# Kernel optimization log

Hardware: AMD Instinct MI355X
Metric: run time of the kernel (lower is better)

The kernel has to match this reference:

```python
import jax, jax.numpy as jnp
import numpy as np

B, N, C_IN, C_OUT, HID = 2, 512, 16, 16, 64


def setup_inputs() -> dict:
    key = jax.random.key(0)
    ks = jax.random.split(key, 6)
    return {
        "features": jax.random.normal(ks[0], (B, N, C_IN), dtype=jnp.float32),
        "geometry": jax.random.normal(ks[1], (B, N, 3), dtype=jnp.float32),
        "W1": jax.random.normal(ks[2], (HID, 4), dtype=jnp.float32) * 0.5,
        "b1": jax.random.normal(ks[3], (HID,), dtype=jnp.float32) * 0.1,
        "W2": jax.random.normal(ks[4], (C_OUT * C_IN, HID), dtype=jnp.float32) * 0.1,
        "b2": jax.random.normal(ks[5], (C_OUT * C_IN,), dtype=jnp.float32) * 0.1,
    }


def reference(features, geometry, W1, b1, W2, b2):
    # rb = geometry.unsqueeze(1) -> [z,1,b,xyz]; ra = geometry.unsqueeze(2) -> [z,a,1,xyz]
    rel = geometry[:, None, :, :] - geometry[:, :, None, :]  # [z, a, b, 3] = rb - ra
    # kernel network: MLP on (rel, |rel|) -> [z, a, b, C_out, C_in]
    r2 = jnp.sum(rel * rel, axis=-1, keepdims=True)
    norm = jnp.sqrt(r2 + 1e-12)                              # differentiable at 0
    feat = jnp.concatenate([rel, norm], axis=-1)             # [z, a, b, 4]
    h = jax.nn.gelu(jnp.einsum('zabf,hf->zabh', feat, W1) + b1)
    k = (jnp.einsum('zabh,oh->zabo', h, W2) + b2)            # [z, a, b, C_out*C_in]
    z, a, b = k.shape[:3]
    k = k.reshape(z, a, b, C_OUT, C_IN)
    # contraction: torch.einsum('zabij,zbj->zabi')
    return jnp.einsum('zabij,zbj->zabi', k, features)
```

## Files before the change

### kernel.cpp

```cpp
#include <hip/hip_runtime.h>

#define NQ   512
#define CI   16
#define CO   16
#define HIDN 64

typedef __attribute__((ext_vector_type(8))) short bf16x8;
typedef __attribute__((ext_vector_type(4))) float f32x4;
typedef __attribute__((ext_vector_type(4))) unsigned u32x4;
typedef __attribute__((ext_vector_type(2))) unsigned u32x2;

__device__ __forceinline__ unsigned cvt_pk_bf16(float a, float b) {
    unsigned r;
    asm("v_cvt_pk_bf16_f32 %0, %1, %2" : "=v"(r) : "v"(a), "v"(b));
    return r;
}

__global__ __launch_bounds__(256, 4) void fused_mfma_kernel(
    const float* __restrict__ features,
    const float* __restrict__ geometry,
    const float* __restrict__ W1,
    const float* __restrict__ b1,
    const float* __restrict__ W2,
    const float* __restrict__ b2,
    float* __restrict__ out)
{
    __shared__ __attribute__((aligned(16))) unsigned short Mhi[CO * HIDN];
    __shared__ __attribute__((aligned(16))) unsigned short Mlo[CO * HIDN];
    __shared__ __attribute__((aligned(16))) float W1_sm[HIDN * 4];
    __shared__ float b1_sm[HIDN];
    __shared__ float c_sm[CO];
    __shared__ float f_sm[CI];

    const int bid = blockIdx.x;
    const int zb  = bid >> 1;
    const int a0  = (bid & 1) << 8;
    const int z   = zb >> 9;
    const int b   = zb & 511;
    const int tid = threadIdx.x;

    W1_sm[tid] = W1[tid];
    if (tid < HIDN) b1_sm[tid] = b1[tid];
    if (tid < CI)   f_sm[tid]  = features[zb * CI + tid];
    __syncthreads();

    const int wv    = tid >> 6;
    const int lane  = tid & 63;
    const int col   = lane & 15;
    const int g     = lane >> 4;
    const int abase = a0 + wv * 64;

    const float gbx = geometry[(z * NQ + b) * 3 + 0];
    const float gby = geometry[(z * NQ + b) * 3 + 1];
    const float gbz = geometry[(z * NQ + b) * 3 + 2];
    float rel[4][4];
    #pragma unroll
    for (int t = 0; t < 4; ++t) {
        const float* ga = geometry + (size_t)(z * NQ + abase + t * 16 + col) * 3;
        float rx = gbx - ga[0], ry = gby - ga[1], rz = gbz - ga[2];
        rel[t][0] = rx; rel[t][1] = ry; rel[t][2] = rz;
        rel[t][3] = sqrtf(fmaf(rx, rx, fmaf(ry, ry, rz * rz)) + 1e-12f);
    }

    {
        const int i  = tid >> 4;
        const int k4 = (tid & 15) << 2;
        f32x4 m = {0.f, 0.f, 0.f, 0.f};
        #pragma unroll
        for (int j = 0; j < CI; ++j) {
            const f32x4 w2 = *reinterpret_cast<const f32x4*>(&W2[(i * CI + j) * HIDN + k4]);
            const float fj = f_sm[j];
            #pragma unroll
            for (int p = 0; p < 4; ++p) m[p] = fmaf(fj, w2[p], m[p]);
        }
        const unsigned h0 = cvt_pk_bf16(m[0], m[1]);
        const unsigned h1 = cvt_pk_bf16(m[2], m[3]);
        const float f0 = __builtin_bit_cast(float, h0 << 16);
        const float f1 = __builtin_bit_cast(float, h0 & 0xffff0000u);
        const float f2 = __builtin_bit_cast(float, h1 << 16);
        const float f3 = __builtin_bit_cast(float, h1 & 0xffff0000u);
        const unsigned l0 = cvt_pk_bf16(m[0] - f0, m[1] - f1);
        const unsigned l1 = cvt_pk_bf16(m[2] - f2, m[3] - f3);
        const int bir = (k4 << 1) ^ ((i & 7) << 4);
        *reinterpret_cast<u32x2*>(reinterpret_cast<char*>(Mhi) + i * 128 + bir) = (u32x2){h0, h1};
        *reinterpret_cast<u32x2*>(reinterpret_cast<char*>(Mlo) + i * 128 + bir) = (u32x2){l0, l1};
    }
    if (tid < CO) {
        float acc = 0.f;
        #pragma unroll
        for (int j = 0; j < CI; ++j)
            acc = fmaf(f_sm[j], b2[tid * CI + j], acc);
        c_sm[tid] = acc;
    }
    __syncthreads();

    bf16x8 Af[2][2];
    #pragma unroll
    for (int kc = 0; kc < 2; ++kc) {
        const int bir = (kc * 64 + g * 16) ^ ((col & 7) << 4);
        Af[0][kc] = *reinterpret_cast<const bf16x8*>(reinterpret_cast<const char*>(Mhi) + col * 128 + bir);
        Af[1][kc] = *reinterpret_cast<const bf16x8*>(reinterpret_cast<const char*>(Mlo) + col * 128 + bir);
    }

    f32x4 cin;
    #pragma unroll
    for (int r = 0; r < 4; ++r) cin[r] = c_sm[g * 4 + r];
    f32x4 acc[4];
    #pragma unroll
    for (int t = 0; t < 4; ++t) acc[t] = cin;

    #pragma unroll
    for (int kc = 0; kc < 2; ++kc) {
        f32x4 w[8]; float bbias[8];
        #pragma unroll
        for (int j = 0; j < 8; ++j) {
            const int h = kc * 32 + g * 8 + j;
            w[j]     = *reinterpret_cast<const f32x4*>(&W1_sm[h * 4]);
            bbias[j] = b1_sm[h];
        }
        #pragma unroll
        for (int t = 0; t < 4; ++t) {
            float hv[8];
            #pragma unroll
            for (int j = 0; j < 8; ++j) {
                float x = bbias[j];
                x = fmaf(rel[t][0], w[j][0], x);
                x = fmaf(rel[t][1], w[j][1], x);
                x = fmaf(rel[t][2], w[j][2], x);
                x = fmaf(rel[t][3], w[j][3], x);
                float q = fmaf(x * x, 0.044715f, 1.0f);
                float e = __builtin_amdgcn_exp2f((-2.3022082f * x) * q);
                hv[j]   = x * __builtin_amdgcn_rcpf(1.0f + e);
            }
            u32x4 up;
            #pragma unroll
            for (int p = 0; p < 4; ++p)
                up[p] = cvt_pk_bf16(hv[2 * p], hv[2 * p + 1]);
            const bf16x8 av = __builtin_bit_cast(bf16x8, up);
            acc[t] = __builtin_amdgcn_mfma_f32_16x16x32_bf16(Af[0][kc], av, acc[t], 0, 0, 0);
            acc[t] = __builtin_amdgcn_mfma_f32_16x16x32_bf16(Af[1][kc], av, acc[t], 0, 0, 0);
        }
    }

    #pragma unroll
    for (int t = 0; t < 4; ++t) {
        float* op = out + (((size_t)(z * NQ + abase + t * 16 + col)) * NQ + b) * CO + g * 4;
        *reinterpret_cast<f32x4*>(op) = acc[t];
    }
}

extern "C" void kernel_launch(void* const* d_in, const int* in_sizes, int n_in,
                              void* d_out, int out_size, void* d_ws, size_t ws_size,
                              hipStream_t stream) {
    const float* features = (const float*)d_in[0];
    const float* geometry = (const float*)d_in[1];
    const float* W1       = (const float*)d_in[2];
    const float* b1       = (const float*)d_in[3];
    const float* W2       = (const float*)d_in[4];
    const float* b2       = (const float*)d_in[5];
    float* out = (float*)d_out;

    fused_mfma_kernel<<<2048, 256, 0, stream>>>(
        features, geometry, W1, b1, W2, b2, out);
}
```

Baseline: 25.33 us.

## Split into M-precompute kernel and a/b-tiled apply kernel with LDS-transposed stores

A separate kernel now computes the per-(z,b) features·W2 matrix, split into hi/lo bf16 parts, plus the bias term, and writes them to workspace. A second kernel tiles over 16 a by 64 b and loads M per b from global memory. It stages MFMA results through LDS so each output row is written as contiguous runs along b, replacing the strided 16-byte stores of the old kernel. The trade-off is an extra launch, workspace traffic, and M being re-read from cache by every a-tile. The old fused kernel remains as a fallback when workspace is too small.

```diff
diff --git a/kernel.cpp b/kernel.cpp
--- a/kernel.cpp
+++ b/kernel.cpp
@@ -7,22 +7,157 @@
 
 typedef __attribute__((ext_vector_type(8))) short bf16x8;
 typedef __attribute__((ext_vector_type(4))) float f32x4;
-typedef __attribute__((ext_vector_type(4))) unsigned u32x4;
-typedef __attribute__((ext_vector_type(2))) unsigned u32x2;
+typedef __attribute__((ext_vector_type(2))) float f32x2;
 
 __device__ __forceinline__ unsigned cvt_pk_bf16(float a, float b) {
     unsigned r;
     asm("v_cvt_pk_bf16_f32 %0, %1, %2" : "=v"(r) : "v"(a), "v"(b));
     return r;
 }
-
-__global__ __launch_bounds__(256, 4) void fused_mfma_kernel(
+__device__ __forceinline__ unsigned short f32_to_bf16_rne(float v) {
+    unsigned u = __builtin_bit_cast(unsigned, v);
+    u += 0x7fffu + ((u >> 16) & 1u);
+    return (unsigned short)(u >> 16);
+}
+
+__global__ __launch_bounds__(256) void compute_M_kernel(
     const float* __restrict__ features,
+    const float* __restrict__ W2,
+    const float* __restrict__ b2,
+    unsigned short* __restrict__ Mbf,
+    float* __restrict__ Cws)
+{
+    const int zb  = blockIdx.x;
+    const int tid = threadIdx.x;
+
+    float f[CI];
+    #pragma unroll
+    for (int j = 0; j < CI; ++j) f[j] = features[zb * CI + j];
+
+    #pragma unroll
+    for (int e = 0; e < 4; ++e) {
+        int idx = tid + e * 256;
+        int i   = idx >> 6;
+        int k   = idx & 63;
+        float acc = 0.f;
+        #pragma unroll
+        for (int j = 0; j < CI; ++j)
+            acc = fmaf(f[j], W2[(i * CI + j) * HIDN + k], acc);
+        unsigned short hi = f32_to_bf16_rne(acc);
+        float hf = __builtin_bit_cast(float, (unsigned)hi << 16);
+        unsigned short lo = f32_to_bf16_rne(acc - hf);
+        Mbf[(size_t)zb * 2048 + idx]        = hi;
+        Mbf[(size_t)zb * 2048 + 1024 + idx] = lo;
+    }
+    if (tid < CO) {
+        float acc = 0.f;
+        #pragma unroll
+        for (int j = 0; j < CI; ++j)
+            acc = fmaf(f[j], b2[tid * CI + j], acc);
+        Cws[zb * CO + tid] = acc;
+    }
+}
+
+__global__ __launch_bounds__(512, 4) void apply_transpose_kernel(
     const float* __restrict__ geometry,
     const float* __restrict__ W1,
     const float* __restrict__ b1,
-    const float* __restrict__ W2,
-    const float* __restrict__ b2,
+    const unsigned short* __restrict__ Mbf,
+    const float* __restrict__ Cws,
+    float* __restrict__ out)
+{
+    __shared__ float tbuf[8 * 8 * 306];
+
+    const int bid  = blockIdx.x;
+    const int z    = bid >> 8;
+    const int a_t  = (bid >> 3) & 31;
+    const int b_t  = bid & 7;
+    const int tid  = threadIdx.x;
+    const int wv   = tid >> 6;
+    const int lane = tid & 63;
+    const int col  = lane & 15;
+    const int g    = lane >> 4;
+
+    const int a0 = a_t * 16;
+    const int bq = b_t * 64 + wv * 8;
+
+    float* wbuf = tbuf + wv * (8 * 306);
+
+    const float* ga = geometry + (size_t)(z * NQ + a0 + col) * 3;
+    const float gax = ga[0], gay = ga[1], gaz = ga[2];
+
+    float bb[16];
+    #pragma unroll
+    for (int kc = 0; kc < 2; ++kc)
+        #pragma unroll
+        for (int j = 0; j < 8; ++j)
+            bb[kc * 8 + j] = b1[kc * 32 + g * 8 + j];
+
+    #pragma unroll 1
+    for (int bl = 0; bl < 8; ++bl) {
+        const int b = bq + bl;
+        const float gbx = geometry[(z * NQ + b) * 3 + 0];
+        const float gby = geometry[(z * NQ + b) * 3 + 1];
+        const float gbz = geometry[(z * NQ + b) * 3 + 2];
+        const float rx = gbx - gax, ry = gby - gay, rz = gbz - gaz;
+        const float nrm = sqrtf(fmaf(rx, rx, fmaf(ry, ry, rz * rz)) + 1e-12f);
+
+        const unsigned short* Mzb = Mbf + (size_t)(z * NQ + b) * 2048;
+        bf16x8 Af[2][2];
+        #pragma unroll
+        for (int part = 0; part < 2; ++part)
+            #pragma unroll
+            for (int kc = 0; kc < 2; ++kc)
+                Af[part][kc] = *reinterpret_cast<const bf16x8*>(
+                    Mzb + part * 1024 + col * 64 + kc * 32 + g * 8);
+
+        f32x4 acc = *reinterpret_cast<const f32x4*>(Cws + (z * NQ + b) * CO + g * 4);
+
+        #pragma unroll
+        for (int kc = 0; kc < 2; ++kc) {
+            float hv[8];
+            #pragma unroll
+            for (int j = 0; j < 8; ++j) {
+                const int h = kc * 32 + g * 8 + j;
+                const f32x4 w = *reinterpret_cast<const f32x4*>(W1 + h * 4);
+                float x = bb[kc * 8 + j];
+                x = fmaf(rx,  w[0], x);
+                x = fmaf(ry,  w[1], x);
+                x = fmaf(rz,  w[2], x);
+                x = fmaf(nrm, w[3], x);
+                float q = fmaf(x * x, 0.044715f, 1.0f);
+                float e = __builtin_amdgcn_exp2f((-2.3022082f * x) * q);
+                hv[j]   = x * __builtin_amdgcn_rcpf(1.0f + e);
+            }
+            unsigned up0 = cvt_pk_bf16(hv[0], hv[1]);
+            unsigned up1 = cvt_pk_bf16(hv[2], hv[3]);
+            unsigned up2 = cvt_pk_bf16(hv[4], hv[5]);
+            unsigned up3 = cvt_pk_bf16(hv[6], hv[7]);
+            __attribute__((ext_vector_type(4))) unsigned up = {up0, up1, up2, up3};
+            const bf16x8 av = __builtin_bit_cast(bf16x8, up);
+            acc = __builtin_amdgcn_mfma_f32_16x16x32_bf16(Af[0][kc], av, acc, 0, 0, 0);
+            acc = __builtin_amdgcn_mfma_f32_16x16x32_bf16(Af[1][kc], av, acc, 0, 0, 0);
+        }
+
+        const int base = bl * 306 + col * 18 + g * 4;
+        *reinterpret_cast<f32x2*>(&wbuf[base])     = (f32x2){acc[0], acc[1]};
+        *reinterpret_cast<f32x2*>(&wbuf[base + 2]) = (f32x2){acc[2], acc[3]};
+    }
+
+    const int bp = lane >> 3;
+    const int ip = lane & 7;
+    #pragma unroll
+    for (int ar = 0; ar < 16; ++ar) {
+        const f32x2 v = *reinterpret_cast<const f32x2*>(&wbuf[bp * 306 + ar * 18 + ip * 2]);
+        float* op = out + (((size_t)(z * NQ + a0 + ar)) * NQ + bq) * CO + lane * 2;
+        *reinterpret_cast<f32x2*>(op) = v;
+    }
+}
+
+__global__ __launch_bounds__(256, 4) void fused_mfma_kernel(
+    const float* __restrict__ features, const float* __restrict__ geometry,
+    const float* __restrict__ W1, const float* __restrict__ b1,
+    const float* __restrict__ W2, const float* __restrict__ b2,
     float* __restrict__ out)
 {
     __shared__ __attribute__((aligned(16))) unsigned short Mhi[CO * HIDN];
@@ -82,6 +217,7 @@
         const unsigned l0 = cvt_pk_bf16(m[0] - f0, m[1] - f1);
         const unsigned l1 = cvt_pk_bf16(m[2] - f2, m[3] - f3);
         const int bir = (k4 << 1) ^ ((i & 7) << 4);
+        typedef __attribute__((ext_vector_type(2))) unsigned u32x2;
         *reinterpret_cast<u32x2*>(reinterpret_cast<char*>(Mhi) + i * 128 + bir) = (u32x2){h0, h1};
         *reinterpret_cast<u32x2*>(reinterpret_cast<char*>(Mlo) + i * 128 + bir) = (u32x2){l0, l1};
     }
@@ -132,6 +268,7 @@
                 float e = __builtin_amdgcn_exp2f((-2.3022082f * x) * q);
                 hv[j]   = x * __builtin_amdgcn_rcpf(1.0f + e);
             }
+            typedef __attribute__((ext_vector_type(4))) unsigned u32x4;
             u32x4 up;
             #pragma unroll
             for (int p = 0; p < 4; ++p)
@@ -160,6 +297,16 @@
     const float* b2       = (const float*)d_in[5];
     float* out = (float*)d_out;
 
-    fused_mfma_kernel<<<2048, 256, 0, stream>>>(
-        features, geometry, W1, b1, W2, b2, out);
-}
+    const size_t needM = (size_t)1024 * 2048 * sizeof(unsigned short);
+    const size_t needC = (size_t)1024 * CO * sizeof(float);
+    if (ws_size >= needM + needC) {
+        unsigned short* Mbf = (unsigned short*)d_ws;
+        float* Cws = (float*)((char*)d_ws + needM);
+        compute_M_kernel<<<1024, 256, 0, stream>>>(features, W2, b2, Mbf, Cws);
+        apply_transpose_kernel<<<512, 512, 0, stream>>>(
+            geometry, W1, b1, Mbf, Cws, out);
+    } else {
+        fused_mfma_kernel<<<2048, 256, 0, stream>>>(
+            features, geometry, W1, b1, W2, b2, out);
+    }
+}
```

Result: slower. 41.25 us (+62.9%).
